# Performance work log

Hardware: AMD Instinct MI355X
Metric: run time of the kernel (lower is better)

Reference implementation:

```python
import jax, jax.numpy as jnp
import numpy as np

# dims
B, T, D = 32, 64, 32          # batch of trajectories, time steps, state_dim
S = 64                        # loss_sample_size
J = 16                        # max_jumps
R = 8                         # max_rejection_attempts
W = 64                        # drift MLP width
PW = 64                       # tilting (phi) MLP width
ALPHA, TAU, SIGMA = 1.2, 0.1, 0.05
RATE1 = (1.0 / ALPHA) * TAU ** (-ALPHA)   # total_prior_jump_rate per unit time
MAX_EXP = 80.0
EPS = 1e-6


def _trunc_stable(k, shape):
    """Truncated stable jumps: tau * (1-u)^(-1/alpha)."""
    u = jax.random.uniform(k, shape, dtype=jnp.float32)
    return TAU * jnp.power(1.0 - u, -1.0 / ALPHA)


def setup_inputs() -> dict:
    key = jax.random.key(0)
    ks = jax.random.split(key, 8)

    def w(k, shape, scale):
        return (scale * jax.random.normal(k, shape)).astype(jnp.float32)

    return {
        "state_init": w(ks[0], (B, D), 0.1),
        "time_sequence": jnp.arange(T, dtype=jnp.float32) * 0.01,
        "dW1": w(ks[1], (D + 1, W), (D + 1) ** -0.5),
        "db1": jnp.zeros((W,), jnp.float32),
        "dW2": w(ks[2], (W, W), W ** -0.5),
        "db2": jnp.zeros((W,), jnp.float32),
        "dW3": w(ks[3], (W, D), 0.1 * W ** -0.5),
        "db3": jnp.zeros((D,), jnp.float32),
        "diff_log": jnp.zeros((D,), jnp.float32),
        "pW1": w(ks[4], (1, PW), 0.5),
        "pb1": jnp.zeros((PW,), jnp.float32),
        "pW2": w(ks[5], (PW, PW), PW ** -0.5),
        "pb2": jnp.zeros((PW,), jnp.float32),
        "pW3": w(ks[6], (PW, 2 * D), 0.1 * PW ** -0.5),
        "pb3": jnp.zeros((2 * D,), jnp.float32),
    }


def _forward(state_init, time_sequence, dW1, db1, dW2, db2, dW3, db3,
             diff_log, pW1, pb1, pW2, pb2, pW3, pb3):
    diff_scale = jax.nn.softplus(diff_log)  # DiagonalScaleFactor, (D,)

    def drift(t, X):  # NeuralNetFunction MLP over [t, x]
        tcol = jnp.full((X.shape[0], 1), t, dtype=X.dtype)
        h = jnp.tanh(jnp.concatenate([tcol, X], axis=1) @ dW1 + db1)
        h = jnp.tanh(h @ dW2 + db2)
        return h @ dW3 + db3  # (B, D)

    def phi_coeffs(t):  # QuadraticNeuralPotential coefficients A_t (<0), B_t
        h = jnp.tanh(t * pW1[0] + pb1)
        h = jnp.tanh(h @ pW2 + pb2)
        out = h @ pW3 + pb3  # (2D,)
        return -jax.nn.softplus(out[:D]), out[D:]

    def step(carry, t):
        X, past_t, key = carry  # X: (B, D)
        dt = t - past_t
        key, k_stab, k_pois, k_rej, k_gauss = jax.random.split(key, 5)

        # tilting weights from truncated stable proposal jumps
        raw = _trunc_stable(k_stab, (B, S, D))
        scaled = diff_scale * raw                       # (B,S,D)
        A_t, B_t = phi_coeffs(t)                        # (D,), (D,)
        K1 = 2.0 * A_t * X + B_t                        # (B,D)
        quad = A_t * scaled ** 2
        lin = K1[:, None, :] * scaled
        log_H = MAX_EXP * jnp.tanh((quad + lin) / MAX_EXP)
        nlog_H = MAX_EXP * jnp.tanh((quad - lin) / MAX_EXP)
        tilt_w = jnp.exp(log_H) + jnp.exp(nlog_H)       # (B,S,D)
        tq = jnp.nanquantile(tilt_w, 0.95, axis=1)      # (B,D)
        tilt = jnp.nanmean(jnp.minimum(tilt_w, tq[:, None, :]), axis=1)  # (B,D)
        total_rate = tilt * RATE1 * dt
        n_jumps = jax.random.poisson(k_pois, total_rate)  # (B,D) int

        # rejection-sampled mixing variable (vectorized over B and J)
        Mb = jnp.exp(-K1 ** 2 / (4.0 * A_t))[:, None, :]  # envelope, (B,1,D)

        def attempt(c, _):
            r, acc, k = c
            k, kp, ka = jax.random.split(k, 3)
            r_prop = _trunc_stable(kp, (B, J, D))
            denom = jnp.maximum(1.0 - 2.0 * A_t * r_prop ** 2 * SIGMA ** 2, EPS)
            C = jnp.exp(K1[:, None, :] ** 2 * r_prop ** 2 * SIGMA ** 2 / (2.0 * denom)) / jnp.sqrt(denom)
            p = jnp.minimum(C / Mb, 1.0)
            u = jax.random.uniform(ka, (B, J, D))
            new = (u < p) & ~acc
            return (jnp.where(new, r_prop, r), acc | new, k), None

        init = (jnp.full((B, J, D), TAU, jnp.float32),
                jnp.zeros((B, J, D), bool), k_rej)
        (r_mix, _, _), _ = jax.lax.scan(attempt, init, None, length=R)

        # conditional Gaussian given mixing variable
        K2 = A_t - 1.0 / (2.0 * r_mix ** 2 * SIGMA ** 2)  # (B,J,D)
        K2s = jnp.where(K2 < -EPS, K2, -EPS)
        mean = -K1[:, None, :] / (2.0 * K2s)
        var = -1.0 / (2.0 * K2s)
        cond = mean + jnp.sqrt(var) * jax.random.normal(k_gauss, (B, J, D))

        mask = jnp.arange(J)[None, :, None] < n_jumps[:, None, :]  # (B,J,D)
        soj = jnp.nansum(cond * mask, axis=1)                       # (B,D)
        clip = 50.0 * SIGMA
        soj = clip * jnp.tanh(soj / clip)

        X = X + drift(t, X) * dt + diff_scale * soj
        return (X, t, key), X

    key0 = jax.random.key(42)
    _, path = jax.lax.scan(step, (state_init, time_sequence[0], key0), time_sequence)
    return path  # (T, B, D)


def reference(state_init, time_sequence, dW1, db1, dW2, db2, dW3, db3,
              diff_log, pW1, pb1, pW2, pb2, pW3, pb3):
    return _forward(state_init, time_sequence, dW1, db1, dW2, db2, dW3, db3,
                    diff_log, pW1, pb1, pW2, pb2, pW3, pb3)
```

## Files before the change

### kernel.cpp

```cpp
#include <hip/hip_runtime.h>
#include <cstdint>
#include <math.h>

#pragma clang fp contract(off)

#define DEV __device__ __forceinline__

struct U2 { unsigned a, b; };

DEV unsigned rotl32(unsigned v, int d) { return (v << d) | (v >> (32 - d)); }

DEV U2 tf2(unsigned k0, unsigned k1, unsigned x0, unsigned x1) {
  unsigned ks2 = k0 ^ k1 ^ 0x1BD11BDAu;
  x0 += k0; x1 += k1;
#define TFR(r) { x0 += x1; x1 = rotl32(x1, r); x1 ^= x0; }
  TFR(13) TFR(15) TFR(26) TFR(6)
  x0 += k1; x1 += ks2 + 1u;
  TFR(17) TFR(29) TFR(16) TFR(24)
  x0 += ks2; x1 += k0 + 2u;
  TFR(13) TFR(15) TFR(26) TFR(6)
  x0 += k0; x1 += k1 + 3u;
  TFR(17) TFR(29) TFR(16) TFR(24)
  x0 += k1; x1 += ks2 + 4u;
  TFR(13) TFR(15) TFR(26) TFR(6)
// ... 76 lines not shown
  q = q * x2 + 2.26843463243900e-03f;
  q = q * x2 + 4.89352518554385e-03f;
  float r = p / q;
  return (fabsf(x) < 0.0004f) ? x : r;
}

DEV float sqrt_cr(float x) { return (float)sqrt((double)x); }

DEV float xla_log1p(float x) {
  float fl = xla_log(x + 1.0f);
  float fs = ((-0.5f) * x + 1.0f) * x;
  return (fabsf(x) < 1e-4f) ? fs : fl;
}

DEV float softplus_ref(float x) {
  float amax = fmaxf(x, 0.0f);
  return amax + xla_log1p(xla_exp(-fabsf(x)));
}

DEV float xla_erfinv(float x) {
  float w = -xla_log1p(-(x * x));
  bool lt = w < 5.0f;
  float wa = lt ? (w - 2.5f) : (sqrt_cr(w) - 3.0f);
  float p;
  if (lt) {
    p = 2.81022636e-08f;
    p = p * wa + 3.43273939e-07f;
    p = p * wa + -3.5233877e-06f;
    p = p * wa + -4.39150654e-06f;
    p = p * wa + 0.00021858087f;
    p = p * wa + -0.00125372503f;
    p = p * wa + -0.00417768164f;
    p = p * wa + 0.246640727f;
    p = p * wa + 1.50140941f;
  } else {
    p = -0.000200214257f;
    p = p * wa + 0.000100950558f;
    p = p * wa + 0.00134934322f;
    p = p * wa + -0.00367342844f;
    p = p * wa + 0.00573950773f;
    p = p * wa + -0.0076224613f;
    p = p * wa + 0.00943887047f;
    p = p * wa + 1.00167406f;
    p = p * wa + 2.83297682f;
  }
  return p * x;
}

DEV float powm(float x) {
  const double e = (double)((float)(-1.0 / 1.2));
  return (float)pow((double)x, e);
}

#define Bn 32
#define Tn 64
#define Dn 32
#define Sn 64
#define Jn 16
#define SIG2F  0.0025000000000000005f
#define RATE1F 13.207443270509278f
#define LO_N  -0.99999994039535522f
#define SQRT2F 1.4142135623730951f

#define OFF_A    0
#define OFF_B    2048
#define OFF_DS   4096
#define OFF_KEYS 4128
#define OFF_KA   4640
#define OFF_KP   5664
#define OFF_SUB  6688
#define OFF_RAW  16384
#define OFF_RP   4210688
#define OFF_LK   12599296
#define OFF_U2   13713408
#define OFF_Z    22102016
#define WS_FLOATS_M1 13713408
#define WS_FLOATS_M2 23150592
#define NRAW 4194304
#define NRP  8388608
#define NU2  8388608
#define NZ   1048576
#define NLK  65536

__global__ void __launch_bounds__(64) key_kernel(unsigned* __restrict__ wsu) {
  __shared__ unsigned lk[64][2];
  int t = threadIdx.x;
  if (t == 0) {
    unsigned k0 = 0u, k1 = 42u;
    for (int i = 0; i < 64; ++i) {
      lk[i][0] = k0; lk[i][1] = k1;
      U2 c0 = tf2(k0, k1, 0u, 0u);
      k0 = c0.a; k1 = c0.b;
    }
  }
  __syncthreads();
  unsigned k0 = lk[t][0], k1 = lk[t][1];
  U2 c1 = tf2(k0, k1, 0u, 1u);
  U2 c2 = tf2(k0, k1, 0u, 2u);
  U2 c3 = tf2(k0, k1, 0u, 3u);
  U2 c4 = tf2(k0, k1, 0u, 4u);
  wsu[OFF_KEYS + t * 8 + 0] = c1.a; wsu[OFF_KEYS + t * 8 + 1] = c1.b;
  wsu[OFF_KEYS + t * 8 + 2] = c2.a; wsu[OFF_KEYS + t * 8 + 3] = c2.b;
  wsu[OFF_KEYS + t * 8 + 4] = c3.a; wsu[OFF_KEYS + t * 8 + 5] = c3.b;
  wsu[OFF_KEYS + t * 8 + 6] = c4.a; wsu[OFF_KEYS + t * 8 + 7] = c4.b;
  unsigned a0 = c3.a, a1 = c3.b;
  for (int a = 0; a < 8; ++a) {
    U2 kp = tf2(a0, a1, 0u, 1u);
    U2 ka = tf2(a0, a1, 0u, 2u);
    U2 nx = tf2(a0, a1, 0u, 0u);
    wsu[OFF_KP + (t * 8 + a) * 2 + 0] = kp.a; wsu[OFF_KP + (t * 8 + a) * 2 + 1] = kp.b;
    wsu[OFF_KA + (t * 8 + a) * 2 + 0] = ka.a; wsu[OFF_KA + (t * 8 + a) * 2 + 1] = ka.b;
    a0 = nx.a; a1 = nx.b;
  }
  unsigned r0 = c2.a, r1 = c2.b;
  for (int k = 0; k < 17; ++k) {
    U2 sub = tf2(r0, r1, 0u, 1u);
    U2 nx  = tf2(r0, r1, 0u, 0u);
    wsu[OFF_SUB + (t * 17 + k) * 2 + 0] = sub.a; wsu[OFF_SUB + (t * 17 + k) * 2 + 1] = sub.b;
    r0 = nx.a; r1 = nx.b;
  }
}

template <bool FULL>
__global__ void __launch_bounds__(256) stable_kernel(const unsigned* __restrict__ wsu,
                                                     float* __restrict__ ws) {
  const int NTOT = FULL ? (NRAW + NRP + NU2 + NZ + NLK) : (NRAW + NRP);
  int stride = gridDim.x * blockDim.x;
  for (int idx = blockIdx.x * blockDim.x + threadIdx.x; idx < NTOT; idx += stride) {
    if (idx < NRAW) {
      int t = idx >> 16;
      int b = (idx >> 11) & 31;
      int e = idx & 2047;
      unsigned k0 = wsu[OFF_KEYS + t * 8 + 0], k1 = wsu[OFF_KEYS + t * 8 + 1];
      float u = u01(rbits(k0, k1, (unsigned)(b * 2048 + e)));
      ws[OFF_RAW + idx] = 0.1f * powm(1.0f - u);
    } else if (idx < NRAW + NRP) {
      int i2 = idx - NRAW;
      int t = i2 >> 17;
      int b = (i2 >> 12) & 31;
      int jd = (i2 >> 3) & 511;
      int a = i2 & 7;
      unsigned k0 = wsu[OFF_KP + (t * 8 + a) * 2], k1 = wsu[OFF_KP + (t * 8 + a) * 2 + 1];
      float u1 = u01(rbits(k0, k1, (unsigned)(b * 512 + jd)));
      ws[OFF_RP + i2] = 0.1f * powm(1.0f - u1);
    } else if (FULL && idx < NRAW + NRP + NU2) {
      int i3 = idx - (NRAW + NRP);
      int t = i3 >> 17;
      int b = (i3 >> 12) & 31;
      int jd = (i3 >> 3) & 511;
      int a = i3 & 7;
      unsigned k0 = wsu[OFF_KA + (t * 8 + a) * 2], k1 = wsu[OFF_KA + (t * 8 + a) * 2 + 1];
      ws[OFF_U2 + i3] = u01(rbits(k0, k1, (unsigned)(b * 512 + jd)));
    } else if (FULL && idx < NRAW + NRP + NU2 + NZ) {
      int i4 = idx - (NRAW + NRP + NU2);
      int t = i4 >> 14;
      int b = (i4 >> 9) & 31;
      int jd = i4 & 511;
      unsigned k0 = wsu[OFF_KEYS + t * 8 + 6], k1 = wsu[OFF_KEYS + t * 8 + 7];
      float fz = u01(rbits(k0, k1, (unsigned)(b * 512 + jd)));
      float un = fmaxf(LO_N, fz * 2.0f + LO_N);
      ws[OFF_Z + i4] = SQRT2F * xla_erfinv(un);
    } else if (FULL) {
      int i5 = idx - (NRAW + NRP + NU2 + NZ);
      int t = i5 >> 10;
      int b = (i5 >> 5) & 31;
      int d = i5 & 31;
      float L = 0.0f;
      for (int k = 0; k < 17; ++k) {
        unsigned s0 = wsu[OFF_SUB + (t * 17 + k) * 2], s1 = wsu[OFF_SUB + (t * 17 + k) * 2 + 1];
        float u = u01(rbits(s0, s1, (unsigned)(b * 32 + d)));
        L = L + xla_log(u);
        ws[OFF_LK + ((t * 32 + b) * 17 + k) * 32 + d] = L;
      }
    }
  }
}

__global__ void __launch_bounds__(256) lk_kernel(const unsigned* __restrict__ wsu,
                                                 float* __restrict__ ws) {
  int idx = blockIdx.x * 256 + threadIdx.x;
  int t = idx >> 10;
  int b = (idx >> 5) & 31;
  int d = idx & 31;
  float L = 0.0f;
  for (int k = 0; k < 17; ++k) {
    unsigned s0 = wsu[OFF_SUB + (t * 17 + k) * 2], s1 = wsu[OFF_SUB + (t * 17 + k) * 2 + 1];
    float u = u01(rbits(s0, s1, (unsigned)(b * 32 + d)));
    L = L + xla_log(u);
    ws[OFF_LK + ((t * 32 + b) * 17 + k) * 32 + d] = L;
  }
}

__global__ void __launch_bounds__(64) phi_kernel(
    const float* __restrict__ tseq,
    const float* __restrict__ pW1, const float* __restrict__ pb1,
    const float* __restrict__ pW2, const float* __restrict__ pb2,
    const float* __restrict__ pW3, const float* __restrict__ pb3,
    const float* __restrict__ diff_log, float* __restrict__ ws) {
  __shared__ float h1[64], h2[64];
  int t = blockIdx.x, w = threadIdx.x;
  float tv = tseq[t];
  h1[w] = xla_tanh(tv * pW1[w] + pb1[w]);
  __syncthreads();
  float acc = 0.0f;
  for (int k = 0; k < 64; ++k) acc = fmaf(h1[k], pW2[k * 64 + w], acc);
  acc = acc + pb2[w];
  h2[w] = xla_tanh(acc);
  __syncthreads();
  acc = 0.0f;
  for (int k = 0; k < 64; ++k) acc = fmaf(h2[k], pW3[k * 64 + w], acc);
  acc = acc + pb3[w];
  if (w < 32) ws[OFF_A + t * 32 + w] = -softplus_ref(acc);
  else        ws[OFF_B + t * 32 + (w - 32)] = acc;
  if (t == 0 && w < 32) ws[OFF_DS + w] = softplus_ref(diff_log[w]);
}

__global__ void __launch_bounds__(1024) sim2_kernel(
    const float* __restrict__ state_init, const float* __restrict__ tseq,
    const float* __restrict__ gW1, const float* __restrict__ gb1,
    const float* __restrict__ gW2, const float* __restrict__ gb2,
    const float* __restrict__ gW3, const float* __restrict__ gb3,
    const float* __restrict__ ws, float* __restrict__ out) {
  const int b = blockIdx.x;
  const int tid = threadIdx.x;

  __shared__ float sW1[33 * 64], sB1[64], sW2[64 * 64], sB2[64], sW3[64 * 32], sB3[32];
  __shared__ float sTseq[64];
  __shared__ float sX[32], sK1[32], sA[32], sMb[32], sDrift[32], sDs[32];
  __shared__ int   sNj[32];
  __shared__ float sH1[64], sH2[64];
  __shared__ float sTilt[32 * 65];
  __shared__ float sRp[4096];
  __shared__ float sCond[512];

  for (int i = tid; i < 33 * 64; i += 1024) sW1[i] = gW1[i];
  for (int i = tid; i < 64 * 64; i += 1024) sW2[i] = gW2[i];
  for (int i = tid; i < 64 * 32; i += 1024) sW3[i] = gW3[i];
  if (tid < 64) { sB1[tid] = gb1[tid]; sB2[tid] = gb2[tid]; sTseq[tid] = tseq[tid]; }
  if (tid < 32) { sB3[tid] = gb3[tid]; sX[tid] = state_init[b * 32 + tid]; sDs[tid] = ws[OFF_DS + tid]; }
  __syncthreads();

  if (tid < 32) {
// ... 146 lines not shown
        int n = 0;
#pragma unroll
        for (int k = 0; k < 17; ++k) n += (lk[k] > negl) ? 1 : 0;
        sNj[tid] = n;
      }
    }
    __syncthreads();

    if (tid < 512) {
      int jd = tid, d = jd & 31;
      float r = 0.1f;
      bool found = false;
#pragma unroll
      for (int a = 0; a < 8; ++a) {
        float v = sRp[jd * 8 + a];
        if (!found && v > 0.0f) { r = v; found = true; }
      }
      float z = cZ;
      float A = sA[d], K1 = sK1[d];
      float t2 = (2.0f * (r * r)) * SIG2F;
      float K2 = A - 1.0f / t2;
      float K2s = (K2 < -1e-6f) ? K2 : -1e-6f;
      float mean = (-K1) / (2.0f * K2s);
      float var = (-1.0f) / (2.0f * K2s);
      float cond = mean + sqrt_cr(var) * z;
      bool mk = (jd >> 5) < sNj[d];
      sCond[jd] = cond * (mk ? 1.0f : 0.0f);
    }
    __syncthreads();

    if (tid < 32) {
      int d = tid;
      float soj = 0.0f;
      for (int j = 0; j < 16; ++j) soj = soj + sCond[j * 32 + d];
      soj = 2.5f * xla_tanh(soj / 2.5f);
      float Xn = (sX[d] + sDrift[d] * dt) + sDs[d] * soj;
      sX[d] = Xn;
      out[ti * 1024 + b * 32 + d] = Xn;
      sA[d] = nA;
      float K1n = (2.0f * nA) * Xn + nB;
      sK1[d] = K1n;
      sMb[d] = xla_exp((-(K1n * K1n)) / (4.0f * nA));
    }
    __syncthreads();

    cRaw0 = nRaw0; cRaw1 = nRaw1; cRaw2 = nRaw2;
#pragma unroll
    for (int q = 0; q < 4; ++q) { cRp[q] = nRp[q]; cU2[q] = nU2[q]; }
    cZ = nZ;
    past_t = t;
  }
}

template <bool PRE>
__global__ void __launch_bounds__(1024) sim_kernel(
    const float* __restrict__ state_init, const float* __restrict__ tseq,
    const float* __restrict__ gW1, const float* __restrict__ gb1,
    const float* __restrict__ gW2, const float* __restrict__ gb2,
    const float* __restrict__ gW3, const float* __restrict__ gb3,
    const float* __restrict__ ws, const unsigned* __restrict__ wsu,
    float* __restrict__ out) {
  const int b = blockIdx.x;
  const int tid = threadIdx.x;

  __shared__ float sW1[33 * 64], sB1[64], sW2[64 * 64], sB2[64], sW3[64 * 32], sB3[32];
  __shared__ float sTseq[64];
  __shared__ float sX[32], sK1[32], sA[32], sMb[32], sDrift[32], sDs[32];
  __shared__ int   sNj[32];
  __shared__ float sH1[64], sH2[64];
  __shared__ float sTilt[32 * 65];
  __shared__ float sCond[512];
  __shared__ float sRp[4096];
  __shared__ unsigned char sFlag[4096];
  __shared__ unsigned sKeyStep[8], sKaF[16], sKpF[16], sSubF[34];

  for (int i = tid; i < 33 * 64; i += 1024) sW1[i] = gW1[i];
  for (int i = tid; i < 64 * 64; i += 1024) sW2[i] = gW2[i];
  for (int i = tid; i < 64 * 32; i += 1024) sW3[i] = gW3[i];
  if (tid < 64) { sB1[tid] = gb1[tid]; sB2[tid] = gb2[tid]; sTseq[tid] = tseq[tid]; }
  if (tid < 32) { sB3[tid] = gb3[tid]; sX[tid] = state_init[b * 32 + tid]; sDs[tid] = ws[OFF_DS + tid]; }
  __syncthreads();

  float past_t = sTseq[0];

  for (int ti = 0; ti < Tn; ++ti) {
    float t = sTseq[ti];
    float dt = t - past_t;

    float pRaw0 = 0.0f, pRaw1 = 0.0f, pRp[4] = {0, 0, 0, 0};
    float pLk[17];
    float pA = 0.0f, pBc = 0.0f;
    if (PRE) {
      int rawbase = (ti * 32 + b) * 2048;
      pRaw0 = ws[OFF_RAW + rawbase + tid];
      pRaw1 = ws[OFF_RAW + rawbase + tid + 1024];
      int rpbase = (ti * 32 + b) * 4096;
#pragma unroll
      for (int q = 0; q < 4; ++q) pRp[q] = ws[OFF_RP + rpbase + tid + q * 1024];
    }
    if (tid < 32) {
      if (PRE) {
#pragma unroll
        for (int k = 0; k < 17; ++k) pLk[k] = ws[OFF_LK + ((ti * 32 + b) * 17 + k) * 32 + tid];
      }
      pA  = ws[OFF_A + ti * 32 + tid];
      pBc = ws[OFF_B + ti * 32 + tid];
    }
    if (tid < 8)  sKeyStep[tid] = wsu[OFF_KEYS + ti * 8 + tid];
    if (tid >= 8  && tid < 24) sKaF[tid - 8]  = wsu[OFF_KA + ti * 16 + (tid - 8)];
    if (tid >= 24 && tid < 40) sKpF[tid - 24] = wsu[OFF_KP + ti * 16 + (tid - 24)];
    if (tid >= 40 && tid < 74) sSubF[tid - 40] = wsu[OFF_SUB + ti * 34 + (tid - 40)];

    if (tid < 64) {
      float acc = 0.0f;
      acc = fmaf(t, sW1[tid], acc);
      for (int k = 1; k < 33; ++k) acc = fmaf(sX[k - 1], sW1[k * 64 + tid], acc);
      acc = acc + sB1[tid];
      sH1[tid] = xla_tanh(acc);
    }
    __syncthreads();
    if (tid < 64) {
      float acc = 0.0f;
      for (int k = 0; k < 64; ++k) acc = fmaf(sH1[k], sW2[k * 64 + tid], acc);
      acc = acc + sB2[tid];
      sH2[tid] = xla_tanh(acc);
    }
    __syncthreads();
    if (tid < 32) {
      float acc = 0.0f;
      for (int k = 0; k < 64; ++k) acc = fmaf(sH2[k], sW3[k * 32 + tid], acc);
      acc = acc + sB3[tid];
      sDrift[tid] = acc;
      sA[tid] = pA;
      float K1 = (2.0f * pA) * sX[tid] + pBc;
      sK1[tid] = K1;
      sMb[tid] = xla_exp((-(K1 * K1)) / (4.0f * pA));
    }
    __syncthreads();

    {
      int d = tid & 31;
      float K1 = sK1[d], A = sA[d], dsv = sDs[d];
      float raw0, raw1;
      if (PRE) { raw0 = pRaw0; raw1 = pRaw1; }
      else {
        unsigned ks0 = sKeyStep[0], ks1 = sKeyStep[1];
        raw0 = 0.1f * powm(1.0f - u01(rbits(ks0, ks1, (unsigned)(b * 2048 + tid))));
        raw1 = 0.1f * powm(1.0f - u01(rbits(ks0, ks1, (unsigned)(b * 2048 + tid + 1024))));
      }
      float scaled = dsv * raw0;
      float quad = A * (scaled * scaled);
      float lin = K1 * scaled;
      float lh = 80.0f * xla_tanh((quad + lin) / 80.0f);
      float nh = 80.0f * xla_tanh((quad - lin) / 80.0f);
      sTilt[d * 65 + (tid >> 5)] = xla_exp(lh) + xla_exp(nh);
      scaled = dsv * raw1;
      quad = A * (scaled * scaled);
      lin = K1 * scaled;
      lh = 80.0f * xla_tanh((quad + lin) / 80.0f);
      nh = 80.0f * xla_tanh((quad - lin) / 80.0f);
      sTilt[d * 65 + ((tid + 1024) >> 5)] = xla_exp(lh) + xla_exp(nh);
    }
    __syncthreads();

    {
      int wv = tid >> 6, lane = tid & 63;
      float vo0 = sTilt[wv * 65 + lane];
      float vo1 = sTilt[(wv + 16) * 65 + lane];
      float v0 = vo0, v1 = vo1;
      for (int k = 2; k <= 64; k <<= 1)
        for (int j = k >> 1; j > 0; j >>= 1) {
          float o0 = __shfl_xor(v0, j, 64);
          float o1 = __shfl_xor(v1, j, 64);
          bool keepmin = (((lane & j) == 0) == ((lane & k) == 0));
          v0 = keepmin ? fminf(v0, o0) : fmaxf(v0, o0);
          v1 = keepmin ? fminf(v1, o1) : fmaxf(v1, o1);
        }
      float qv = 0.95f * 63.0f;
      float hw = qv - 59.0f;
      float lw = 1.0f - hw;
      float s59 = __shfl(v0, 59, 64), s60 = __shfl(v0, 60, 64);
      float tq0 = s59 * lw + s60 * hw;
      s59 = __shfl(v1, 59, 64); s60 = __shfl(v1, 60, 64);
      float tq1 = s59 * lw + s60 * hw;
      sTilt[wv * 65 + lane] = fminf(vo0, tq0);
      sTilt[(wv + 16) * 65 + lane] = fminf(vo1, tq1);
    }
    __syncthreads();

    {
#pragma unroll
      for (int q = 0; q < 4; ++q) {
        int tau = tid + q * 1024;
        int jd = tau >> 3, a = tau & 7, d = jd & 31;
        float A = sA[d], K1 = sK1[d];
        float K1sq = K1 * K1;
        float rp;
        if (PRE) rp = pRp[q];
        else rp = 0.1f * powm(1.0f - u01(rbits(sKpF[a * 2], sKpF[a * 2 + 1], (unsigned)(b * 512 + jd))));
        float rp2 = rp * rp;
        float den = fmaxf(1.0f - ((2.0f * A) * rp2) * SIG2F, 1e-6f);
        float Cv = xla_exp(((K1sq * rp2) * SIG2F) / (2.0f * den)) / sqrt_cr(den);
        float p = fminf(Cv / sMb[d], 1.0f);
        float u2 = u01(rbits(sKaF[a * 2], sKaF[a * 2 + 1], (unsigned)(b * 512 + jd)));
        sFlag[tau] = (u2 < p) ? (unsigned char)1 : (unsigned char)0;
        sRp[tau] = rp;
      }
      if (tid < 32) {
        float sum = 0.0f;
        for (int s = 0; s < 64; ++s) sum = sum + sTilt[tid * 65 + s];
        float tilt = sum / 64.0f;
        float lam = (tilt * RATE1F) * dt;
        float negl = -lam;
        int n = 0;
        if (PRE) {
#pragma unroll
          for (int k = 0; k < 17; ++k) n += (pLk[k] > negl) ? 1 : 0;
        } else {
          float L = 0.0f;
          for (int k = 0; k < 17; ++k) {
            float u = u01(rbits(sSubF[k * 2], sSubF[k * 2 + 1], (unsigned)(b * 32 + tid)));
            L = L + xla_log(u);
            n += (L > negl) ? 1 : 0;
          }
        }
        sNj[tid] = n;
      }
    }
    __syncthreads();

    if (tid < 512) {
      int jd = tid, d = jd & 31;
      float r = 0.1f;
      bool found = false;
#pragma unroll
      for (int a = 0; a < 8; ++a) {
        if (!found && sFlag[jd * 8 + a]) { r = sRp[jd * 8 + a]; found = true; }
      }
      float fz = u01(rbits(sKeyStep[6], sKeyStep[7], (unsigned)(b * 512 + jd)));
      float un = fmaxf(LO_N, fz * 2.0f + LO_N);
      float z = SQRT2F * xla_erfinv(un);
      float A = sA[d], K1 = sK1[d];
      float t2 = (2.0f * (r * r)) * SIG2F;
      float K2 = A - 1.0f / t2;
      float K2s = (K2 < -1e-6f) ? K2 : -1e-6f;
      float mean = (-K1) / (2.0f * K2s);
      float var = (-1.0f) / (2.0f * K2s);
      float cond = mean + sqrt_cr(var) * z;
      bool mk = (jd >> 5) < sNj[d];
      sCond[jd] = cond * (mk ? 1.0f : 0.0f);
    }
    __syncthreads();

    if (tid < 32) {
      int d = tid;
      float soj = 0.0f;
      for (int j = 0; j < 16; ++j) soj = soj + sCond[j * 32 + d];
      soj = 2.5f * xla_tanh(soj / 2.5f);
      float Xn = (sX[d] + sDrift[d] * dt) + sDs[d] * soj;
      sX[d] = Xn;
      out[ti * 1024 + b * 32 + d] = Xn;
    }
    __syncthreads();
    past_t = t;
  }
}

extern "C" void kernel_launch(void* const* d_in, const int* in_sizes, int n_in,
                              void* d_out, int out_size, void* d_ws, size_t ws_size,
                              hipStream_t stream) {
  const float* state_init = (const float*)d_in[0];
  const float* tseq       = (const float*)d_in[1];
  const float* dW1        = (const float*)d_in[2];
  const float* db1        = (const float*)d_in[3];
  const float* dW2        = (const float*)d_in[4];
  const float* db2        = (const float*)d_in[5];
  const float* dW3        = (const float*)d_in[6];
  const float* db3        = (const float*)d_in[7];
  const float* diff_log   = (const float*)d_in[8];
  const float* pW1        = (const float*)d_in[9];
  const float* pb1        = (const float*)d_in[10];
  const float* pW2        = (const float*)d_in[11];
  const float* pb2        = (const float*)d_in[12];
  const float* pW3        = (const float*)d_in[13];
  const float* pb3        = (const float*)d_in[14];
  float* ws = (float*)d_ws;
  unsigned* wsu = (unsigned*)d_ws;

  bool m2 = ws_size >= (size_t)WS_FLOATS_M2 * 4;
  bool m1 = ws_size >= (size_t)WS_FLOATS_M1 * 4;

  key_kernel<<<1, 64, 0, stream>>>(wsu);
  phi_kernel<<<64, 64, 0, stream>>>(tseq, pW1, pb1, pW2, pb2, pW3, pb3, diff_log, ws);
  if (m2) {
    stable_kernel<true><<<4096, 256, 0, stream>>>(wsu, ws);
    sim2_kernel<<<32, 1024, 0, stream>>>(state_init, tseq, dW1, db1, dW2, db2,
                                         dW3, db3, ws, (float*)d_out);
  } else if (m1) {
    stable_kernel<false><<<4096, 256, 0, stream>>>(wsu, ws);
    lk_kernel<<<256, 256, 0, stream>>>(wsu, ws);
    sim_kernel<true><<<32, 1024, 0, stream>>>(state_init, tseq, dW1, db1, dW2, db2,
                                              dW3, db3, ws, wsu, (float*)d_out);
  } else {
    sim_kernel<false><<<32, 1024, 0, stream>>>(state_init, tseq, dW1, db1, dW2, db2,
                                               dW3, db3, ws, wsu, (float*)d_out);
  }
}
```

Before: 713.5 us.

## Fuse key, phi, RNG precompute and simulation into one cooperative producer-consumer kernel

Replaces the separate key, phi, stable-precompute and simulation launches with a single cooperative kernel. Blocks 0-31 run the per-trajectory simulation, and 224 producer blocks generate the random draws one time step at a time. Per-step atomic counters with acquire/release fences let the simulation start step t as soon as that step's data exists, instead of waiting for all precompute. Producers also precompute derived quantities (scaled jumps, quadratic terms, rp², sqrt denominators), and the sort-based quantile becomes a top-5 max-selection. The cost is spin-waiting, a larger workspace, and a dependence on all blocks being co-resident, with a fallback to the old path if the cooperative launch fails.

```diff
diff --git a/kernel.cpp b/kernel.cpp
--- a/kernel.cpp
+++ b/kernel.cpp
@@ -152,15 +152,409 @@
   return (float)pow((double)x, e);
 }
 
-#define Bn 32
-#define Tn 64
-#define Dn 32
-#define Sn 64
-#define Jn 16
 #define SIG2F  0.0025000000000000005f
 #define RATE1F 13.207443270509278f
 #define LO_N  -0.99999994039535522f
 #define SQRT2F 1.4142135623730951f
+#define Tn 64
+
+#define AGENT __HIP_MEMORY_SCOPE_AGENT
+DEV void spin_ge(const unsigned* p, unsigned target) {
+  while (__hip_atomic_load(p, __ATOMIC_RELAXED, AGENT) < target)
+    __builtin_amdgcn_s_sleep(2);
+  __builtin_amdgcn_fence(__ATOMIC_ACQUIRE, "agent");
+}
+DEV void release_add(unsigned* p) {
+  __builtin_amdgcn_fence(__ATOMIC_RELEASE, "agent");
+  __hip_atomic_fetch_add(p, 1u, __ATOMIC_RELAXED, AGENT);
+}
+
+#define F_A      0
+#define F_B      2048
+#define F_DS     4096
+#define F_KEYS   4128
+#define F_KA     4640
+#define F_KP     5664
+#define F_SUB    6688
+#define F_CNT    8864
+#define F_SCALED 16384
+#define F_QUAD   4210688
+#define F_RP2    8404992
+#define F_SQ     16793600
+#define F_U2     25182208
+#define F_Z      33570816
+#define F_LK     34619392
+#define F_END    35733504
+#define NPROD 224
+#define UNITS_PER_SLAB 214016
+#define CHUNK 956
+
+__global__ void __launch_bounds__(1024) fat_kernel(
+    const float* __restrict__ state_init, const float* __restrict__ tseq,
+    const float* __restrict__ gW1, const float* __restrict__ gb1,
+    const float* __restrict__ gW2, const float* __restrict__ gb2,
+    const float* __restrict__ gW3, const float* __restrict__ gb3,
+    const float* __restrict__ diff_log,
+    const float* __restrict__ pW1, const float* __restrict__ pb1,
+    const float* __restrict__ pW2, const float* __restrict__ pb2,
+    const float* __restrict__ pW3, const float* __restrict__ pb3,
+    float* ws, float* __restrict__ out) {
+  unsigned* wsu = (unsigned*)ws;
+  unsigned* cnt = &wsu[F_CNT];
+  unsigned* initFlag = &wsu[F_CNT + 64];
+  const int bid = blockIdx.x;
+  const int tid = threadIdx.x;
+
+  __shared__ float sW1[33 * 64], sB1[64], sW2[64 * 64], sB2[64], sW3[64 * 32], sB3[32];
+  __shared__ float sTseq[64];
+  __shared__ float sX[32], sK1[32], sA[32], sMb[32], sDrift[32], sDs[32];
+  __shared__ int   sNj[32];
+  __shared__ float sH1[64], sH2[64];
+  __shared__ float sTilt[32 * 65];
+  __shared__ float sSel[4096];
+  __shared__ float sCond[512];
+  __shared__ unsigned sChainK[128];
+
+  if (bid >= 32) {
+    const int pid = bid - 32;
+    if (pid == 0) {
+      if (tid == 0) {
+        unsigned k0 = 0u, k1 = 42u;
+        for (int i = 0; i < 64; ++i) {
+          sChainK[i * 2] = k0; sChainK[i * 2 + 1] = k1;
+          U2 c0 = tf2(k0, k1, 0u, 0u);
+          k0 = c0.a; k1 = c0.b;
+        }
+      }
+      __syncthreads();
+      if (tid < 64) {
+        unsigned k0 = sChainK[tid * 2], k1 = sChainK[tid * 2 + 1];
+        U2 c1 = tf2(k0, k1, 0u, 1u);
+        U2 c2 = tf2(k0, k1, 0u, 2u);
+        U2 c3 = tf2(k0, k1, 0u, 3u);
+        U2 c4 = tf2(k0, k1, 0u, 4u);
+        wsu[F_KEYS + tid * 8 + 0] = c1.a; wsu[F_KEYS + tid * 8 + 1] = c1.b;
+        wsu[F_KEYS + tid * 8 + 2] = c2.a; wsu[F_KEYS + tid * 8 + 3] = c2.b;
+        wsu[F_KEYS + tid * 8 + 4] = c3.a; wsu[F_KEYS + tid * 8 + 5] = c3.b;
+        wsu[F_KEYS + tid * 8 + 6] = c4.a; wsu[F_KEYS + tid * 8 + 7] = c4.b;
+        unsigned a0 = c3.a, a1 = c3.b;
+        for (int a = 0; a < 8; ++a) {
+          U2 kp = tf2(a0, a1, 0u, 1u);
+          U2 ka = tf2(a0, a1, 0u, 2u);
+          U2 nx = tf2(a0, a1, 0u, 0u);
+          wsu[F_KP + (tid * 8 + a) * 2 + 0] = kp.a; wsu[F_KP + (tid * 8 + a) * 2 + 1] = kp.b;
+          wsu[F_KA + (tid * 8 + a) * 2 + 0] = ka.a; wsu[F_KA + (tid * 8 + a) * 2 + 1] = ka.b;
+          a0 = nx.a; a1 = nx.b;
+        }
+        unsigned r0 = c2.a, r1 = c2.b;
+        for (int k = 0; k < 17; ++k) {
+          U2 sub = tf2(r0, r1, 0u, 1u);
+          U2 nx  = tf2(r0, r1, 0u, 0u);
+          wsu[F_SUB + (tid * 17 + k) * 2 + 0] = sub.a; wsu[F_SUB + (tid * 17 + k) * 2 + 1] = sub.b;
+          r0 = nx.a; r1 = nx.b;
+        }
+      }
+      __syncthreads();
+      for (int j = tid; j < 4096; j += 1024) {
+        int tt = j >> 6, w_ = j & 63;
+        sSel[j] = xla_tanh(tseq[tt] * pW1[w_] + pb1[w_]);
+      }
+      __syncthreads();
+      for (int j = tid; j < 4096; j += 1024) {
+        int tt = j >> 6, w_ = j & 63;
+        float acc = 0.0f;
+        for (int k = 0; k < 64; ++k) acc = fmaf(sSel[tt * 64 + k], pW2[k * 64 + w_], acc);
+        sW2[j] = xla_tanh(acc + pb2[w_]);
+      }
+      __syncthreads();
+      for (int j = tid; j < 4096; j += 1024) {
+        int tt = j >> 6, o = j & 63;
+        float acc = 0.0f;
+        for (int k = 0; k < 64; ++k) acc = fmaf(sW2[tt * 64 + k], pW3[k * 64 + o], acc);
+        acc = acc + pb3[o];
+        if (o < 32) ws[F_A + tt * 32 + o] = -softplus_ref(acc);
+        else        ws[F_B + tt * 32 + (o - 32)] = acc;
+      }
+      if (tid < 32) ws[F_DS + tid] = softplus_ref(diff_log[tid]);
+      __syncthreads();
+      if (tid == 0) {
+        __builtin_amdgcn_fence(__ATOMIC_RELEASE, "agent");
+        __hip_atomic_store(initFlag, 1u, __ATOMIC_RELAXED, AGENT);
+      }
+    }
+    if (tid == 0) spin_ge(initFlag, 1u);
+    __syncthreads();
+
+    const int u0 = pid * CHUNK;
+    const int u1 = (u0 + CHUNK < UNITS_PER_SLAB) ? (u0 + CHUNK) : UNITS_PER_SLAB;
+    for (int t = 0; t < Tn; ++t) {
+      int u = u0 + tid;
+      if (u < u1) {
+        if (u < 65536) {
+          int b_ = u >> 11, e = u & 2047, d = e & 31;
+          unsigned k0 = wsu[F_KEYS + t * 8 + 0], k1 = wsu[F_KEYS + t * 8 + 1];
+          float uu = u01(rbits(k0, k1, (unsigned)(b_ * 2048 + e)));
+          float raw = 0.1f * powm(1.0f - uu);
+          float scaled = ws[F_DS + d] * raw;
+          float A = ws[F_A + t * 32 + d];
+          ws[F_SCALED + t * 65536 + u] = scaled;
+          ws[F_QUAD   + t * 65536 + u] = A * (scaled * scaled);
+        } else if (u < 196608) {
+          int i = u - 65536;
+          int b_ = i >> 12, jd = (i >> 3) & 511, a = i & 7, d = jd & 31;
+          unsigned p0 = wsu[F_KP + (t * 8 + a) * 2], p1 = wsu[F_KP + (t * 8 + a) * 2 + 1];
+          float rp = 0.1f * powm(1.0f - u01(rbits(p0, p1, (unsigned)(b_ * 512 + jd))));
+          float rp2 = rp * rp;
+          float A = ws[F_A + t * 32 + d];
+          float den = fmaxf(1.0f - ((2.0f * A) * rp2) * SIG2F, 1e-6f);
+          unsigned a0 = wsu[F_KA + (t * 8 + a) * 2], a1 = wsu[F_KA + (t * 8 + a) * 2 + 1];
+          ws[F_RP2 + t * 131072 + i] = rp2;
+          ws[F_SQ  + t * 131072 + i] = sqrt_cr(den);
+          ws[F_U2  + t * 131072 + i] = u01(rbits(a0, a1, (unsigned)(b_ * 512 + jd)));
+        } else if (u < 212992) {
+          int i = u - 196608;
+          int b_ = i >> 9, jd = i & 511;
+          unsigned g0 = wsu[F_KEYS + t * 8 + 6], g1 = wsu[F_KEYS + t * 8 + 7];
+          float fz = u01(rbits(g0, g1, (unsigned)(b_ * 512 + jd)));
+          float un = fmaxf(LO_N, fz * 2.0f + LO_N);
+          ws[F_Z + t * 16384 + i] = SQRT2F * xla_erfinv(un);
+        } else {
+          int i = u - 212992;
+          int b_ = i >> 5, d = i & 31;
+          float L = 0.0f;
+          for (int k = 0; k < 17; ++k) {
+            unsigned s0 = wsu[F_SUB + (t * 17 + k) * 2], s1 = wsu[F_SUB + (t * 17 + k) * 2 + 1];
+            L = L + xla_log(u01(rbits(s0, s1, (unsigned)(b_ * 32 + d))));
+            ws[F_LK + ((t * 32 + b_) * 17 + k) * 32 + d] = L;
+          }
+        }
+      }
+      __syncthreads();
+      if (tid == 0) release_add(&cnt[t]);
+    }
+    return;
+  }
+
+  const int b = bid;
+  for (int i = tid; i < 33 * 64; i += 1024) sW1[i] = gW1[i];
+  for (int i = tid; i < 64 * 64; i += 1024) sW2[i] = gW2[i];
+  for (int i = tid; i < 64 * 32; i += 1024) sW3[i] = gW3[i];
+  if (tid < 64) { sB1[tid] = gb1[tid]; sB2[tid] = gb2[tid]; sTseq[tid] = tseq[tid]; }
+  if (tid < 32) sB3[tid] = gb3[tid];
+  if (tid == 0) spin_ge(initFlag, 1u);
+  __syncthreads();
+  if (tid < 32) {
+    sDs[tid] = ws[F_DS + tid];
+    float X0 = state_init[b * 32 + tid];
+    sX[tid] = X0;
+    float A = ws[F_A + tid], Bv = ws[F_B + tid];
+    sA[tid] = A;
+    float K1 = (2.0f * A) * X0 + Bv;
+    sK1[tid] = K1;
+    sMb[tid] = xla_exp((-(K1 * K1)) / (4.0f * A));
+  }
+  if (tid == 0) spin_ge(&cnt[0], NPROD);
+  __syncthreads();
+
+  const int zi = tid & 511;
+  float cSc0, cSc1, cSc2, cQd0, cQd1, cQd2, cRp2[4], cSq[4], cU2[4], cZ;
+  {
+    int tb = b;
+    cSc0 = ws[F_SCALED + tb * 2048 + tid];
+    cQd0 = ws[F_QUAD + tb * 2048 + tid];
+    cSc1 = (tid < 960) ? ws[F_SCALED + tb * 2048 + 960 + tid] : 0.0f;
+    cQd1 = (tid < 960) ? ws[F_QUAD + tb * 2048 + 960 + tid] : 0.0f;
+    cSc2 = (tid < 128) ? ws[F_SCALED + tb * 2048 + 1920 + tid] : 0.0f;
+    cQd2 = (tid < 128) ? ws[F_QUAD + tb * 2048 + 1920 + tid] : 0.0f;
+#pragma unroll
+    for (int q = 0; q < 4; ++q) {
+      cRp2[q] = ws[F_RP2 + tb * 4096 + tid + q * 1024];
+      cSq[q]  = ws[F_SQ + tb * 4096 + tid + q * 1024];
+      cU2[q]  = ws[F_U2 + tb * 4096 + tid + q * 1024];
+    }
+    cZ = ws[F_Z + tb * 512 + zi];
+  }
+  __syncthreads();
+
+  float past_t = sTseq[0];
+  for (int ti = 0; ti < Tn; ++ti) {
+    float t = sTseq[ti];
+    float dt = t - past_t;
+
+    if (tid >= 960) {
+      int l = tid - 960;
+      float acc = 0.0f;
+      acc = fmaf(t, sW1[l], acc);
+      for (int k = 1; k < 33; ++k) acc = fmaf(sX[k - 1], sW1[k * 64 + l], acc);
+      acc = acc + sB1[l];
+      sH1[l] = xla_tanh(acc);
+      float acc2 = 0.0f;
+      for (int k = 0; k < 64; ++k) acc2 = fmaf(sH1[k], sW2[k * 64 + l], acc2);
+      acc2 = acc2 + sB2[l];
+      sH2[l] = xla_tanh(acc2);
+      if (l < 32) {
+        float a3 = 0.0f;
+        for (int k = 0; k < 64; ++k) a3 = fmaf(sH2[k], sW3[k * 32 + l], a3);
+        sDrift[l] = a3 + sB3[l];
+      }
+    } else {
+      {
+        int d = tid & 31;
+        float lin = sK1[d] * cSc0;
+        float lh = 80.0f * xla_tanh((cQd0 + lin) / 80.0f);
+        float nh = 80.0f * xla_tanh((cQd0 - lin) / 80.0f);
+        sTilt[d * 65 + (tid >> 5)] = xla_exp(lh) + xla_exp(nh);
+      }
+      {
+        int e = tid + 960, d = e & 31;
+        float lin = sK1[d] * cSc1;
+        float lh = 80.0f * xla_tanh((cQd1 + lin) / 80.0f);
+        float nh = 80.0f * xla_tanh((cQd1 - lin) / 80.0f);
+        sTilt[d * 65 + (e >> 5)] = xla_exp(lh) + xla_exp(nh);
+      }
+      if (tid < 128) {
+        int e = 1920 + tid, d = e & 31;
+        float lin = sK1[d] * cSc2;
+        float lh = 80.0f * xla_tanh((cQd2 + lin) / 80.0f);
+        float nh = 80.0f * xla_tanh((cQd2 - lin) / 80.0f);
+        sTilt[d * 65 + (e >> 5)] = xla_exp(lh) + xla_exp(nh);
+      }
+    }
+    __syncthreads();
+
+    {
+      int wv = tid >> 6, lane = tid & 63;
+      float vo0 = sTilt[wv * 65 + lane];
+      float vo1 = sTilt[(wv + 16) * 65 + lane];
+      float w0 = vo0, w1 = vo1;
+      float s0_59 = 0.0f, s0_60 = 0.0f, s1_59 = 0.0f, s1_60 = 0.0f;
+#pragma unroll
+      for (int it = 0; it < 5; ++it) {
+        float m0 = w0, m1 = w1;
+#pragma unroll
+        for (int j = 1; j < 64; j <<= 1) {
+          m0 = fmaxf(m0, __shfl_xor(m0, j, 64));
+          m1 = fmaxf(m1, __shfl_xor(m1, j, 64));
+        }
+        if (it == 3) { s0_60 = m0; s1_60 = m1; }
+        if (it == 4) { s0_59 = m0; s1_59 = m1; }
+        if (it < 4) {
+          unsigned long long b0 = __ballot(w0 == m0);
+          unsigned long long b1 = __ballot(w1 == m1);
+          int l0 = __ffsll(b0) - 1;
+          int l1 = __ffsll(b1) - 1;
+          if (lane == l0) w0 = -1.0f;
+          if (lane == l1) w1 = -1.0f;
+        }
+      }
+      float qv = 0.95f * 63.0f;
+      float hw = qv - 59.0f;
+      float lw = 1.0f - hw;
+      float tq0 = s0_59 * lw + s0_60 * hw;
+      float tq1 = s1_59 * lw + s1_60 * hw;
+      sTilt[wv * 65 + lane] = fminf(vo0, tq0);
+      sTilt[(wv + 16) * 65 + lane] = fminf(vo1, tq1);
+    }
+    __syncthreads();
+
+    {
+      float plk[17];
+      if (tid < 32) {
+#pragma unroll
+        for (int k = 0; k < 17; ++k) plk[k] = ws[F_LK + ((ti * 32 + b) * 17 + k) * 32 + tid];
+      }
+#pragma unroll
+      for (int q = 0; q < 4; ++q) {
+        int tau = tid + q * 1024;
+        int d = (tau >> 3) & 31;
+        float A = sA[d], K1 = sK1[d];
+        float K1sq = K1 * K1;
+        float rp2 = cRp2[q];
+        float den = fmaxf(1.0f - ((2.0f * A) * rp2) * SIG2F, 1e-6f);
+        float Cv = xla_exp(((K1sq * rp2) * SIG2F) / (2.0f * den)) / cSq[q];
+        float p = fminf(Cv / sMb[d], 1.0f);
+        sSel[tau] = (cU2[q] < p) ? rp2 : -rp2;
+      }
+      if (tid < 32) {
+        float sum = 0.0f;
+        for (int s = 0; s < 64; ++s) sum = sum + sTilt[tid * 65 + s];
+        float tilt = sum / 64.0f;
+        float lam = (tilt * RATE1F) * dt;
+        float negl = -lam;
+        int n = 0;
+#pragma unroll
+        for (int k = 0; k < 17; ++k) n += (plk[k] > negl) ? 1 : 0;
+        sNj[tid] = n;
+      }
+    }
+    __syncthreads();
+
+    if (tid < 512) {
+      int jd = tid, d = jd & 31;
+      float rp2sel = 0.1f * 0.1f;
+      bool found = false;
+#pragma unroll
+      for (int a = 0; a < 8; ++a) {
+        float v = sSel[jd * 8 + a];
+        if (!found && v > 0.0f) { rp2sel = v; found = true; }
+      }
+      float A = sA[d], K1 = sK1[d];
+      float t2 = (2.0f * rp2sel) * SIG2F;
+      float K2 = A - 1.0f / t2;
+      float K2s = (K2 < -1e-6f) ? K2 : -1e-6f;
+      float mean = (-K1) / (2.0f * K2s);
+      float var = (-1.0f) / (2.0f * K2s);
+      float cond = mean + sqrt_cr(var) * cZ;
+      bool mk = (jd >> 5) < sNj[d];
+      sCond[jd] = cond * (mk ? 1.0f : 0.0f);
+    } else if (tid == 512 && ti < 63) {
+      spin_ge(&cnt[ti + 1], NPROD);
+    }
+    __syncthreads();
+
+    int tn = (ti < 63) ? ti + 1 : 63;
+    float nSc0, nSc1, nSc2, nQd0, nQd1, nQd2, nRp2[4], nSq[4], nU2[4], nZ;
+    float nA = 0.0f, nB = 0.0f;
+    {
+      int tb = tn * 32 + b;
+      nSc0 = ws[F_SCALED + tb * 2048 + tid];
+      nQd0 = ws[F_QUAD + tb * 2048 + tid];
+      nSc1 = (tid < 960) ? ws[F_SCALED + tb * 2048 + 960 + tid] : 0.0f;
+      nQd1 = (tid < 960) ? ws[F_QUAD + tb * 2048 + 960 + tid] : 0.0f;
+      nSc2 = (tid < 128) ? ws[F_SCALED + tb * 2048 + 1920 + tid] : 0.0f;
+      nQd2 = (tid < 128) ? ws[F_QUAD + tb * 2048 + 1920 + tid] : 0.0f;
+#pragma unroll
+      for (int q = 0; q < 4; ++q) {
+        nRp2[q] = ws[F_RP2 + tb * 4096 + tid + q * 1024];
+        nSq[q]  = ws[F_SQ + tb * 4096 + tid + q * 1024];
+        nU2[q]  = ws[F_U2 + tb * 4096 + tid + q * 1024];
+      }
+      nZ = ws[F_Z + tb * 512 + zi];
+      if (tid < 32) { nA = ws[F_A + tn * 32 + tid]; nB = ws[F_B + tn * 32 + tid]; }
+    }
+    if (tid < 32) {
+      int d = tid;
+      float soj = 0.0f;
+      for (int j = 0; j < 16; ++j) soj = soj + sCond[j * 32 + d];
+      soj = 2.5f * xla_tanh(soj / 2.5f);
+      float Xn = (sX[d] + sDrift[d] * dt) + sDs[d] * soj;
+      sX[d] = Xn;
+      out[ti * 1024 + b * 32 + d] = Xn;
+      sA[d] = nA;
+      float K1n = (2.0f * nA) * Xn + nB;
+      sK1[d] = K1n;
+      sMb[d] = xla_exp((-(K1n * K1n)) / (4.0f * nA));
+    }
+    __syncthreads();
+
+    cSc0 = nSc0; cSc1 = nSc1; cSc2 = nSc2;
+    cQd0 = nQd0; cQd1 = nQd1; cQd2 = nQd2;
+#pragma unroll
+    for (int q = 0; q < 4; ++q) { cRp2[q] = nRp2[q]; cSq[q] = nSq[q]; cU2[q] = nU2[q]; }
+    cZ = nZ;
+    past_t = t;
+  }
+}
 
 #define OFF_A    0
 #define OFF_B    2048
@@ -174,7 +568,6 @@
 #define OFF_LK   12599296
 #define OFF_U2   13713408
 #define OFF_Z    22102016
-#define WS_FLOATS_M1 13713408
 #define WS_FLOATS_M2 23150592
 #define NRAW 4194304
 #define NRP  8388608
@@ -221,10 +614,9 @@
   }
 }
 
-template <bool FULL>
 __global__ void __launch_bounds__(256) stable_kernel(const unsigned* __restrict__ wsu,
                                                      float* __restrict__ ws) {
-  const int NTOT = FULL ? (NRAW + NRP + NU2 + NZ + NLK) : (NRAW + NRP);
+  const int NTOT = NRAW + NRP + NU2 + NZ + NLK;
   int stride = gridDim.x * blockDim.x;
   for (int idx = blockIdx.x * blockDim.x + threadIdx.x; idx < NTOT; idx += stride) {
     if (idx < NRAW) {
@@ -243,7 +635,7 @@
       unsigned k0 = wsu[OFF_KP + (t * 8 + a) * 2], k1 = wsu[OFF_KP + (t * 8 + a) * 2 + 1];
       float u1 = u01(rbits(k0, k1, (unsigned)(b * 512 + jd)));
       ws[OFF_RP + i2] = 0.1f * powm(1.0f - u1);
-    } else if (FULL && idx < NRAW + NRP + NU2) {
+    } else if (idx < NRAW + NRP + NU2) {
       int i3 = idx - (NRAW + NRP);
       int t = i3 >> 17;
       int b = (i3 >> 12) & 31;
@@ -251,7 +643,7 @@
       int a = i3 & 7;
       unsigned k0 = wsu[OFF_KA + (t * 8 + a) * 2], k1 = wsu[OFF_KA + (t * 8 + a) * 2 + 1];
       ws[OFF_U2 + i3] = u01(rbits(k0, k1, (unsigned)(b * 512 + jd)));
-    } else if (FULL && idx < NRAW + NRP + NU2 + NZ) {
+    } else if (idx < NRAW + NRP + NU2 + NZ) {
       int i4 = idx - (NRAW + NRP + NU2);
       int t = i4 >> 14;
       int b = (i4 >> 9) & 31;
@@ -260,7 +652,7 @@
       float fz = u01(rbits(k0, k1, (unsigned)(b * 512 + jd)));
       float un = fmaxf(LO_N, fz * 2.0f + LO_N);
       ws[OFF_Z + i4] = SQRT2F * xla_erfinv(un);
-    } else if (FULL) {
+    } else {
       int i5 = idx - (NRAW + NRP + NU2 + NZ);
       int t = i5 >> 10;
       int b = (i5 >> 5) & 31;
@@ -273,21 +665,6 @@
         ws[OFF_LK + ((t * 32 + b) * 17 + k) * 32 + d] = L;
       }
     }
-  }
-}
-
-__global__ void __launch_bounds__(256) lk_kernel(const unsigned* __restrict__ wsu,
-                                                 float* __restrict__ ws) {
-  int idx = blockIdx.x * 256 + threadIdx.x;
-  int t = idx >> 10;
-  int b = (idx >> 5) & 31;
-  int d = idx & 31;
-  float L = 0.0f;
-  for (int k = 0; k < 17; ++k) {
-    unsigned s0 = wsu[OFF_SUB + (t * 17 + k) * 2], s1 = wsu[OFF_SUB + (t * 17 + k) * 2 + 1];
-    float u = u01(rbits(s0, s1, (unsigned)(b * 32 + d)));
-    L = L + xla_log(u);
-    ws[OFF_LK + ((t * 32 + b) * 17 + k) * 32 + d] = L;
   }
 }
 
@@ -540,220 +917,6 @@
   }
 }
 
-template <bool PRE>
-__global__ void __launch_bounds__(1024) sim_kernel(
-    const float* __restrict__ state_init, const float* __restrict__ tseq,
-    const float* __restrict__ gW1, const float* __restrict__ gb1,
-    const float* __restrict__ gW2, const float* __restrict__ gb2,
-    const float* __restrict__ gW3, const float* __restrict__ gb3,
-    const float* __restrict__ ws, const unsigned* __restrict__ wsu,
-    float* __restrict__ out) {
-  const int b = blockIdx.x;
-  const int tid = threadIdx.x;
-
-  __shared__ float sW1[33 * 64], sB1[64], sW2[64 * 64], sB2[64], sW3[64 * 32], sB3[32];
-  __shared__ float sTseq[64];
-  __shared__ float sX[32], sK1[32], sA[32], sMb[32], sDrift[32], sDs[32];
-  __shared__ int   sNj[32];
-  __shared__ float sH1[64], sH2[64];
-  __shared__ float sTilt[32 * 65];
-  __shared__ float sCond[512];
-  __shared__ float sRp[4096];
-  __shared__ unsigned char sFlag[4096];
-  __shared__ unsigned sKeyStep[8], sKaF[16], sKpF[16], sSubF[34];
-
-  for (int i = tid; i < 33 * 64; i += 1024) sW1[i] = gW1[i];
-  for (int i = tid; i < 64 * 64; i += 1024) sW2[i] = gW2[i];
-  for (int i = tid; i < 64 * 32; i += 1024) sW3[i] = gW3[i];
-  if (tid < 64) { sB1[tid] = gb1[tid]; sB2[tid] = gb2[tid]; sTseq[tid] = tseq[tid]; }
-  if (tid < 32) { sB3[tid] = gb3[tid]; sX[tid] = state_init[b * 32 + tid]; sDs[tid] = ws[OFF_DS + tid]; }
-  __syncthreads();
-
-  float past_t = sTseq[0];
-
-  for (int ti = 0; ti < Tn; ++ti) {
-    float t = sTseq[ti];
-    float dt = t - past_t;
-
-    float pRaw0 = 0.0f, pRaw1 = 0.0f, pRp[4] = {0, 0, 0, 0};
-    float pLk[17];
-    float pA = 0.0f, pBc = 0.0f;
-    if (PRE) {
-      int rawbase = (ti * 32 + b) * 2048;
-      pRaw0 = ws[OFF_RAW + rawbase + tid];
-      pRaw1 = ws[OFF_RAW + rawbase + tid + 1024];
-      int rpbase = (ti * 32 + b) * 4096;
-#pragma unroll
-      for (int q = 0; q < 4; ++q) pRp[q] = ws[OFF_RP + rpbase + tid + q * 1024];
-    }
-    if (tid < 32) {
-      if (PRE) {
-#pragma unroll
-        for (int k = 0; k < 17; ++k) pLk[k] = ws[OFF_LK + ((ti * 32 + b) * 17 + k) * 32 + tid];
-      }
-      pA  = ws[OFF_A + ti * 32 + tid];
-      pBc = ws[OFF_B + ti * 32 + tid];
-    }
-    if (tid < 8)  sKeyStep[tid] = wsu[OFF_KEYS + ti * 8 + tid];
-    if (tid >= 8  && tid < 24) sKaF[tid - 8]  = wsu[OFF_KA + ti * 16 + (tid - 8)];
-    if (tid >= 24 && tid < 40) sKpF[tid - 24] = wsu[OFF_KP + ti * 16 + (tid - 24)];
-    if (tid >= 40 && tid < 74) sSubF[tid - 40] = wsu[OFF_SUB + ti * 34 + (tid - 40)];
-
-    if (tid < 64) {
-      float acc = 0.0f;
-      acc = fmaf(t, sW1[tid], acc);
-      for (int k = 1; k < 33; ++k) acc = fmaf(sX[k - 1], sW1[k * 64 + tid], acc);
-      acc = acc + sB1[tid];
-      sH1[tid] = xla_tanh(acc);
-    }
-    __syncthreads();
-    if (tid < 64) {
-      float acc = 0.0f;
-      for (int k = 0; k < 64; ++k) acc = fmaf(sH1[k], sW2[k * 64 + tid], acc);
-      acc = acc + sB2[tid];
-      sH2[tid] = xla_tanh(acc);
-    }
-    __syncthreads();
-    if (tid < 32) {
-      float acc = 0.0f;
-      for (int k = 0; k < 64; ++k) acc = fmaf(sH2[k], sW3[k * 32 + tid], acc);
-      acc = acc + sB3[tid];
-      sDrift[tid] = acc;
-      sA[tid] = pA;
-      float K1 = (2.0f * pA) * sX[tid] + pBc;
-      sK1[tid] = K1;
-      sMb[tid] = xla_exp((-(K1 * K1)) / (4.0f * pA));
-    }
-    __syncthreads();
-
-    {
-      int d = tid & 31;
-      float K1 = sK1[d], A = sA[d], dsv = sDs[d];
-      float raw0, raw1;
-      if (PRE) { raw0 = pRaw0; raw1 = pRaw1; }
-      else {
-        unsigned ks0 = sKeyStep[0], ks1 = sKeyStep[1];
-        raw0 = 0.1f * powm(1.0f - u01(rbits(ks0, ks1, (unsigned)(b * 2048 + tid))));
-        raw1 = 0.1f * powm(1.0f - u01(rbits(ks0, ks1, (unsigned)(b * 2048 + tid + 1024))));
-      }
-      float scaled = dsv * raw0;
-      float quad = A * (scaled * scaled);
-      float lin = K1 * scaled;
-      float lh = 80.0f * xla_tanh((quad + lin) / 80.0f);
-      float nh = 80.0f * xla_tanh((quad - lin) / 80.0f);
-      sTilt[d * 65 + (tid >> 5)] = xla_exp(lh) + xla_exp(nh);
-      scaled = dsv * raw1;
-      quad = A * (scaled * scaled);
-      lin = K1 * scaled;
-      lh = 80.0f * xla_tanh((quad + lin) / 80.0f);
-      nh = 80.0f * xla_tanh((quad - lin) / 80.0f);
-      sTilt[d * 65 + ((tid + 1024) >> 5)] = xla_exp(lh) + xla_exp(nh);
-    }
-    __syncthreads();
-
-    {
-      int wv = tid >> 6, lane = tid & 63;
-      float vo0 = sTilt[wv * 65 + lane];
-      float vo1 = sTilt[(wv + 16) * 65 + lane];
-      float v0 = vo0, v1 = vo1;
-      for (int k = 2; k <= 64; k <<= 1)
-        for (int j = k >> 1; j > 0; j >>= 1) {
-          float o0 = __shfl_xor(v0, j, 64);
-          float o1 = __shfl_xor(v1, j, 64);
-          bool keepmin = (((lane & j) == 0) == ((lane & k) == 0));
-          v0 = keepmin ? fminf(v0, o0) : fmaxf(v0, o0);
-          v1 = keepmin ? fminf(v1, o1) : fmaxf(v1, o1);
-        }
-      float qv = 0.95f * 63.0f;
-      float hw = qv - 59.0f;
-      float lw = 1.0f - hw;
-      float s59 = __shfl(v0, 59, 64), s60 = __shfl(v0, 60, 64);
-      float tq0 = s59 * lw + s60 * hw;
-      s59 = __shfl(v1, 59, 64); s60 = __shfl(v1, 60, 64);
-      float tq1 = s59 * lw + s60 * hw;
-      sTilt[wv * 65 + lane] = fminf(vo0, tq0);
-      sTilt[(wv + 16) * 65 + lane] = fminf(vo1, tq1);
-    }
-    __syncthreads();
-
-    {
-#pragma unroll
-      for (int q = 0; q < 4; ++q) {
-        int tau = tid + q * 1024;
-        int jd = tau >> 3, a = tau & 7, d = jd & 31;
-        float A = sA[d], K1 = sK1[d];
-        float K1sq = K1 * K1;
-        float rp;
-        if (PRE) rp = pRp[q];
-        else rp = 0.1f * powm(1.0f - u01(rbits(sKpF[a * 2], sKpF[a * 2 + 1], (unsigned)(b * 512 + jd))));
-        float rp2 = rp * rp;
-        float den = fmaxf(1.0f - ((2.0f * A) * rp2) * SIG2F, 1e-6f);
-        float Cv = xla_exp(((K1sq * rp2) * SIG2F) / (2.0f * den)) / sqrt_cr(den);
-        float p = fminf(Cv / sMb[d], 1.0f);
-        float u2 = u01(rbits(sKaF[a * 2], sKaF[a * 2 + 1], (unsigned)(b * 512 + jd)));
-        sFlag[tau] = (u2 < p) ? (unsigned char)1 : (unsigned char)0;
-        sRp[tau] = rp;
-      }
-      if (tid < 32) {
-        float sum = 0.0f;
-        for (int s = 0; s < 64; ++s) sum = sum + sTilt[tid * 65 + s];
-        float tilt = sum / 64.0f;
-        float lam = (tilt * RATE1F) * dt;
-        float negl = -lam;
-        int n = 0;
-        if (PRE) {
-#pragma unroll
-          for (int k = 0; k < 17; ++k) n += (pLk[k] > negl) ? 1 : 0;
-        } else {
-          float L = 0.0f;
-          for (int k = 0; k < 17; ++k) {
-            float u = u01(rbits(sSubF[k * 2], sSubF[k * 2 + 1], (unsigned)(b * 32 + tid)));
-            L = L + xla_log(u);
-            n += (L > negl) ? 1 : 0;
-          }
-        }
-        sNj[tid] = n;
-      }
-    }
-    __syncthreads();
-
-    if (tid < 512) {
-      int jd = tid, d = jd & 31;
-      float r = 0.1f;
-      bool found = false;
-#pragma unroll
-      for (int a = 0; a < 8; ++a) {
-        if (!found && sFlag[jd * 8 + a]) { r = sRp[jd * 8 + a]; found = true; }
-      }
-      float fz = u01(rbits(sKeyStep[6], sKeyStep[7], (unsigned)(b * 512 + jd)));
-      float un = fmaxf(LO_N, fz * 2.0f + LO_N);
-      float z = SQRT2F * xla_erfinv(un);
-      float A = sA[d], K1 = sK1[d];
-      float t2 = (2.0f * (r * r)) * SIG2F;
-      float K2 = A - 1.0f / t2;
-      float K2s = (K2 < -1e-6f) ? K2 : -1e-6f;
-      float mean = (-K1) / (2.0f * K2s);
-      float var = (-1.0f) / (2.0f * K2s);
-      float cond = mean + sqrt_cr(var) * z;
-      bool mk = (jd >> 5) < sNj[d];
-      sCond[jd] = cond * (mk ? 1.0f : 0.0f);
-    }
-    __syncthreads();
-
-    if (tid < 32) {
-      int d = tid;
-      float soj = 0.0f;
-      for (int j = 0; j < 16; ++j) soj = soj + sCond[j * 32 + d];
-      soj = 2.5f * xla_tanh(soj / 2.5f);
-      float Xn = (sX[d] + sDrift[d] * dt) + sDs[d] * soj;
-      sX[d] = Xn;
-      out[ti * 1024 + b * 32 + d] = Xn;
-    }
-    __syncthreads();
-    past_t = t;
-  }
-}
-
 extern "C" void kernel_launch(void* const* d_in, const int* in_sizes, int n_in,
                               void* d_out, int out_size, void* d_ws, size_t ws_size,
                               hipStream_t stream) {
@@ -774,23 +937,26 @@
   const float* pb3        = (const float*)d_in[14];
   float* ws = (float*)d_ws;
   unsigned* wsu = (unsigned*)d_ws;
-
-  bool m2 = ws_size >= (size_t)WS_FLOATS_M2 * 4;
-  bool m1 = ws_size >= (size_t)WS_FLOATS_M1 * 4;
-
+  float* outp = (float*)d_out;
+
+  bool fat = ws_size >= (size_t)F_END * 4;
+  if (fat) {
+    (void)hipMemsetAsync((char*)d_ws + (size_t)F_CNT * 4, 0, 65 * 4, stream);
+    void* args[] = {
+      (void*)&state_init, (void*)&tseq,
+      (void*)&dW1, (void*)&db1, (void*)&dW2, (void*)&db2,
+      (void*)&dW3, (void*)&db3, (void*)&diff_log,
+      (void*)&pW1, (void*)&pb1, (void*)&pW2, (void*)&pb2,
+      (void*)&pW3, (void*)&pb3, (void*)&ws, (void*)&outp
+    };
+    hipError_t e = hipLaunchCooperativeKernel((const void*)fat_kernel,
+                                              dim3(256), dim3(1024), args, 0, stream);
+    if (e == hipSuccess) return;
+    (void)hipGetLastError();
+  }
   key_kernel<<<1, 64, 0, stream>>>(wsu);
   phi_kernel<<<64, 64, 0, stream>>>(tseq, pW1, pb1, pW2, pb2, pW3, pb3, diff_log, ws);
-  if (m2) {
-    stable_kernel<true><<<4096, 256, 0, stream>>>(wsu, ws);
-    sim2_kernel<<<32, 1024, 0, stream>>>(state_init, tseq, dW1, db1, dW2, db2,
-                                         dW3, db3, ws, (float*)d_out);
-  } else if (m1) {
-    stable_kernel<false><<<4096, 256, 0, stream>>>(wsu, ws);
-    lk_kernel<<<256, 256, 0, stream>>>(wsu, ws);
-    sim_kernel<true><<<32, 1024, 0, stream>>>(state_init, tseq, dW1, db1, dW2, db2,
-                                              dW3, db3, ws, wsu, (float*)d_out);
-  } else {
-    sim_kernel<false><<<32, 1024, 0, stream>>>(state_init, tseq, dW1, db1, dW2, db2,
-                                               dW3, db3, ws, wsu, (float*)d_out);
-  }
-}
+  stable_kernel<<<4096, 256, 0, stream>>>(wsu, ws);
+  sim2_kernel<<<32, 1024, 0, stream>>>(state_init, tseq, dW1, db1, dW2, db2,
+                                       dW3, db3, ws, outp);
+}
```

Measured after the change: 1.321 ms. 1.85x slower.
